# Performance work log

Hardware: AMD Instinct MI355X
Metric: run time of the kernel (lower is better)

## Reference

```python
import jax, jax.numpy as jnp
import numpy as np

DIM = 256
H_GLOBAL = 8
H_LOCAL = 4  # max(1, num_heads // 2)
WINDOW = 5
HALF = WINDOW // 2
B, S = 4, 2048
EPS = 1e-5


def layer_norm(x, g, b):
    mu = jnp.mean(x, axis=-1, keepdims=True)
    var = jnp.mean(jnp.square(x - mu), axis=-1, keepdims=True)
    return (x - mu) * jax.lax.rsqrt(var + EPS) * g + b


def qkv_proj(x, in_w, in_b):
    qkv = x @ in_w.T + in_b
    return jnp.split(qkv, 3, axis=-1)


def global_mha(x, in_w, in_b, out_w, out_b, nh):
    Bq, Sq, D = x.shape
    hd = D // nh
    q, k, v = qkv_proj(x, in_w, in_b)
    q = q.reshape(Bq, Sq, nh, hd)
    k = k.reshape(Bq, Sq, nh, hd)
    v = v.reshape(Bq, Sq, nh, hd)
    scores = jnp.einsum('bqhd,bkhd->bhqk', q, k) / np.sqrt(hd).astype(np.float32)
    attn = jax.nn.softmax(scores, axis=-1)
    o = jnp.einsum('bhqk,bkhd->bqhd', attn, v).reshape(Bq, Sq, D)
    return o @ out_w.T + out_b


def local_mha(x, in_w, in_b, out_w, out_b, nh):
    # banded sliding-window attention, window = 2*HALF+1, per-query softmax
    Bq, Sq, D = x.shape
    hd = D // nh
    q, k, v = qkv_proj(x, in_w, in_b)
    kp = jnp.pad(k, ((0, 0), (HALF, HALF), (0, 0)))
    vp = jnp.pad(v, ((0, 0), (HALF, HALF), (0, 0)))
    # [B, S, W, D] windows of keys/values around each query position
    k_win = jnp.stack([kp[:, j:j + Sq] for j in range(WINDOW)], axis=2)
    v_win = jnp.stack([vp[:, j:j + Sq] for j in range(WINDOW)], axis=2)
    q = q.reshape(Bq, Sq, nh, hd)
    k_win = k_win.reshape(Bq, Sq, WINDOW, nh, hd)
    v_win = v_win.reshape(Bq, Sq, WINDOW, nh, hd)
    scores = jnp.einsum('bshd,bswhd->bshw', q, k_win) / np.sqrt(hd).astype(np.float32)
    idx = jnp.arange(Sq)[:, None] + jnp.arange(-HALF, HALF + 1)[None, :]  # [S, W]
    valid = (idx >= 0) & (idx < Sq)
    scores = jnp.where(valid[None, :, None, :], scores, -jnp.inf)
    attn = jax.nn.softmax(scores, axis=-1)
    o = jnp.einsum('bshw,bswhd->bshd', attn, v_win).reshape(Bq, Sq, D)
    return o @ out_w.T + out_b


def setup_inputs() -> dict:
    key = jax.random.key(0)
    ks = jax.random.split(key, 8)
    sc = 0.02
    d = DIM
    return {
        'x': jax.random.normal(ks[0], (B, S, d), jnp.float32),
        'g_in_w': jax.random.normal(ks[1], (3 * d, d), jnp.float32) * sc,
        'g_in_b': jnp.zeros((3 * d,), jnp.float32),
        'g_out_w': jax.random.normal(ks[2], (d, d), jnp.float32) * sc,
        'g_out_b': jnp.zeros((d,), jnp.float32),
        't_in_w': jax.random.normal(ks[3], (3 * d, d), jnp.float32) * sc,
        't_in_b': jnp.zeros((3 * d,), jnp.float32),
        't_out_w': jax.random.normal(ks[4], (d, d), jnp.float32) * sc,
        't_out_b': jnp.zeros((d,), jnp.float32),
        'fus_w1': jax.random.normal(ks[5], (2 * d, 2 * d), jnp.float32) * sc,
        'fus_b1': jnp.zeros((2 * d,), jnp.float32),
        'fus_w2': jax.random.normal(ks[6], (d, 2 * d), jnp.float32) * sc,
        'fus_b2': jnp.zeros((d,), jnp.float32),
        'ffn_w1': jax.random.normal(ks[7], (2 * d, d), jnp.float32) * sc,
        'ffn_b1': jnp.zeros((2 * d,), jnp.float32),
        'ffn_w2': jax.random.normal(jax.random.fold_in(key, 9), (d, 2 * d), jnp.float32) * sc,
        'ffn_b2': jnp.zeros((d,), jnp.float32),
        'gn_g': jnp.ones((d,), jnp.float32),
        'gn_b': jnp.zeros((d,), jnp.float32),
        'fn_g': jnp.ones((d,), jnp.float32),
        'fn_b': jnp.zeros((d,), jnp.float32),
    }


def reference(x, g_in_w, g_in_b, g_out_w, g_out_b,
              t_in_w, t_in_b, t_out_w, t_out_b,
              fus_w1, fus_b1, fus_w2, fus_b2,
              ffn_w1, ffn_b1, ffn_w2, ffn_b2,
              gn_g, gn_b, fn_g, fn_b):
    x_global = global_mha(x, g_in_w, g_in_b, g_out_w, g_out_b, H_GLOBAL)
    x_local = local_mha(x, t_in_w, t_in_b, t_out_w, t_out_b, H_LOCAL)
    x_comb = jnp.concatenate([x_global, x_local], axis=-1)
    x_fused = jax.nn.silu(x_comb @ fus_w1.T + fus_b1) @ fus_w2.T + fus_b2
    x = layer_norm(x + x_fused, gn_g, gn_b)
    x_ffn = jax.nn.silu(x @ ffn_w1.T + ffn_b1) @ ffn_w2.T + ffn_b2
    x = layer_norm(x + x_ffn, fn_g, fn_b)
    return x
```

## Files before the change

### kernel.cpp

```cpp
#include <hip/hip_runtime.h>

constexpr int Bb = 4;
constexpr int Ss = 2048;
constexpr int QSTR = 1536;

typedef __bf16 bf16x8 __attribute__((ext_vector_type(8)));
typedef __bf16 bf16x4 __attribute__((ext_vector_type(4)));
typedef float  f32x4  __attribute__((ext_vector_type(4)));

__device__ __forceinline__ void glds16(const void* g, void* l) {
    __builtin_amdgcn_global_load_lds(
        (const __attribute__((address_space(1))) unsigned int*)g,
        (__attribute__((address_space(3))) unsigned int*)l, 16, 0, 0);
}

struct CvtArgs {
    const float* src[9];
    __bf16* dst[9];
    int start[10];
};

__global__ __launch_bounds__(256) void convert_all(CvtArgs a)
{
    int e = 0;
    const int bid = blockIdx.x;
#pragma unroll
    for (int i = 0; i < 8; i++) if (bid >= a.start[i + 1]) e = i + 1;
    const int idx = (bid - a.start[e]) * 256 + threadIdx.x;
    const float* s = a.src[e];
    float4 v0 = *(const float4*)&s[(size_t)idx * 8];
    float4 v1 = *(const float4*)&s[(size_t)idx * 8 + 4];
    bf16x8 o;
    o[0] = (__bf16)v0.x; o[1] = (__bf16)v0.y; o[2] = (__bf16)v0.z; o[3] = (__bf16)v0.w;
    o[4] = (__bf16)v1.x; o[5] = (__bf16)v1.y; o[6] = (__bf16)v1.z; o[7] = (__bf16)v1.w;
    *(bf16x8*)&a.dst[e][(size_t)idx * 8] = o;
}

__global__ __launch_bounds__(256) void gemm128(
    const __bf16* __restrict__ A, const __bf16* __restrict__ W,
    const float* __restrict__ bias, const float* __restrict__ bias2, int bsplit,
    __bf16* __restrict__ C, int K, int ldc)
{
    __shared__ __bf16 As[128 * 64];
    __shared__ __bf16 Ws[128 * 64];
    const int tid = threadIdx.x;
    const int lane = tid & 63;
    const int wv = tid >> 6;
    const int wm = (wv >> 1) * 64;
    const int wn = (wv & 1) * 64;
    const int qrow = lane & 15;
    const int quad = lane >> 4;
    const int n0 = blockIdx.x * 128;
    const int m0 = blockIdx.y * 128;

    f32x4 acc[4][4];
#pragma unroll
    for (int i = 0; i < 4; i++)
#pragma unroll
        for (int j = 0; j < 4; j++) acc[i][j] = {0.f, 0.f, 0.f, 0.f};

    for (int k0 = 0; k0 < K; k0 += 64) {
        __syncthreads();
#pragma unroll
        for (int i = 0; i < 4; i++) {
            const int c = (wv * 4 + i) * 64 + lane;
            const int row = c >> 3, g = c & 7;
            const int gs = (g ^ (row & 7)) * 8;
            glds16(&A[(size_t)(m0 + row) * K + k0 + gs], &As[(wv * 4 + i) * 512]);
            glds16(&W[(size_t)(n0 + row) * K + k0 + gs], &Ws[(wv * 4 + i) * 512]);
        }
        __syncthreads();
#pragma unroll
        for (int ksub = 0; ksub < 2; ksub++) {
            const int gl = ksub * 4 + quad;
            bf16x8 af[4], bf[4];
#pragma unroll
            for (int mi = 0; mi < 4; mi++) {
                const int row = wm + mi * 16 + qrow;
                af[mi] = *(const bf16x8*)&As[row * 64 + (gl ^ (row & 7)) * 8];
            }
#pragma unroll
            for (int ni = 0; ni < 4; ni++) {
                const int row = wn + ni * 16 + qrow;
                bf[ni] = *(const bf16x8*)&Ws[row * 64 + (gl ^ (row & 7)) * 8];
            }
#pragma unroll
            for (int mi = 0; mi < 4; mi++)
#pragma unroll
                for (int ni = 0; ni < 4; ni++)
                    acc[mi][ni] = __builtin_amdgcn_mfma_f32_16x16x32_bf16(
                        af[mi], bf[ni], acc[mi][ni], 0, 0, 0);
        }
    }

    float bz[4];
#pragma unroll
    for (int ni = 0; ni < 4; ni++) {
        const int n = n0 + wn + ni * 16 + qrow;
        bz[ni] = (n < bsplit) ? bias[n] : bias2[n - bsplit];
    }
#pragma unroll
    for (int mi = 0; mi < 4; mi++)
#pragma unroll
        for (int r = 0; r < 4; r++) {
            const int row = m0 + wm + mi * 16 + quad * 4 + r;
#pragma unroll
            for (int ni = 0; ni < 4; ni++) {
                float v = acc[mi][ni][r] + bz[ni];
                C[(size_t)row * ldc + n0 + wn + ni * 16 + qrow] = (__bf16)v;
            }
        }
}

template<bool SILU, bool OUT_BF16>
__global__ __launch_bounds__(256) void gemm_small(
    const __bf16* __restrict__ A0, const __bf16* __restrict__ W0,
    const float* __restrict__ bias0, const __bf16* __restrict__ W1,
    const float* __restrict__ bias1, int nsplit, int aoff1, int coff1,
    void* __restrict__ C, int lda, int K, int ldc)
{
    __shared__ __bf16 As[32 * 128];
    __shared__ __bf16 Ws[64 * 128];
    const int tid = threadIdx.x;
    const int lane = tid & 63;
    const int wv = tid >> 6;
    const int wm = (wv >> 1) * 16;
    const int wn = (wv & 1) * 32;
    const int qrow = lane & 15;
    const int quad = lane >> 4;
    const bool second = (int)blockIdx.x >= nsplit;
    const int bx = second ? (blockIdx.x - nsplit) : blockIdx.x;
    const __bf16* A = second ? (A0 + aoff1) : A0;
    const __bf16* W = second ? W1 : W0;
    const float* bias = second ? bias1 : bias0;
    const int coff = second ? coff1 : 0;
    const int n0 = bx * 64;
    const int m0 = blockIdx.y * 32;

    f32x4 acc[2];
    acc[0] = {0.f, 0.f, 0.f, 0.f};
    acc[1] = {0.f, 0.f, 0.f, 0.f};

    for (int k0 = 0; k0 < K; k0 += 128) {
        __syncthreads();
#pragma unroll
        for (int i = 0; i < 2; i++) {
            const int c = (wv * 2 + i) * 64 + lane;
            const int row = c >> 4, s = c & 15;
            const int gs = ((s & 8) | ((s ^ row) & 7)) * 8;
            glds16(&A[(size_t)(m0 + row) * lda + k0 + gs], &As[(wv * 2 + i) * 512]);
        }
#pragma unroll
        for (int i = 0; i < 4; i++) {
            const int c = (wv * 4 + i) * 64 + lane;
            const int row = c >> 4, s = c & 15;
            const int gs = ((s & 8) | ((s ^ row) & 7)) * 8;
            glds16(&W[(size_t)(n0 + row) * K + k0 + gs], &Ws[(wv * 4 + i) * 512]);
        }
        __syncthreads();
#pragma unroll
        for (int ksub = 0; ksub < 4; ksub++) {
            const int gl = ksub * 4 + quad;
            bf16x8 af, bf[2];
            {
                const int row = wm + qrow;
                const int s = (gl & 8) | ((gl ^ row) & 7);
                af = *(const bf16x8*)&As[row * 128 + s * 8];
            }
#pragma unroll
            for (int ni = 0; ni < 2; ni++) {
                const int row = wn + ni * 16 + qrow;
                const int s = (gl & 8) | ((gl ^ row) & 7);
                bf[ni] = *(const bf16x8*)&Ws[row * 128 + s * 8];
            }
#pragma unroll
            for (int ni = 0; ni < 2; ni++)
                acc[ni] = __builtin_amdgcn_mfma_f32_16x16x32_bf16(
                    af, bf[ni], acc[ni], 0, 0, 0);
        }
    }

    float bz[2];
#pragma unroll
    for (int ni = 0; ni < 2; ni++) bz[ni] = bias[n0 + wn + ni * 16 + qrow];

#pragma unroll
    for (int r = 0; r < 4; r++) {
        const int row = m0 + wm + quad * 4 + r;
#pragma unroll
        for (int ni = 0; ni < 2; ni++) {
            float v = acc[ni][r] + bz[ni];
            if (SILU) v = v / (1.f + __expf(-v));
            const int col = coff + n0 + wn + ni * 16 + qrow;
            if (OUT_BF16)
                ((__bf16*)C)[(size_t)row * ldc + col] = (__bf16)v;
            else
                ((float*)C)[(size_t)row * ldc + col] = v;
        }
    }
}

__global__ __launch_bounds__(512) void attn_fused(
    const __bf16* __restrict__ qkv, __bf16* __restrict__ Op,
    float* __restrict__ Lp, __bf16* __restrict__ acat)
{
    __shared__ __bf16 Kl[2][64 * 32];
    __shared__ __bf16 Vt[2][32 * 72];
    __shared__ __bf16 Pl[8][16 * 72];

    const int t = threadIdx.x;
    const int lane = t & 63;
    const int wv = t >> 6;

    if (blockIdx.x < 1024) {
        const int bid = blockIdx.x;
        const int sp = bid & 1;
        const int qc = (bid >> 1) & 15;
        const int h  = (bid >> 5) & 7;
        const int b  = bid >> 8;
        const int bS = b * Ss;
        const int q0 = qc * 128;

        const int qrow = lane & 15;
        const int quad = lane >> 4;
        const float cQ = 1.4426950408889634f * 0.17677669529663687f;

        bf16x8 qf;
        {
            bf16x8 qraw = *(const bf16x8*)(qkv +
                (size_t)(bS + q0 + wv * 16 + qrow) * QSTR + h * 32 + quad * 8);
#pragma unroll
            for (int i = 0; i < 8; i++) qf[i] = (__bf16)((float)qraw[i] * cQ);
        }
        bf16x8 ones;
#pragma unroll
        for (int i = 0; i < 8; i++) ones[i] = (__bf16)1.0f;

        f32x4 o0 = {0.f, 0.f, 0.f, 0.f};
        f32x4 o1 = {0.f, 0.f, 0.f, 0.f};
        f32x4 lac = {0.f, 0.f, 0.f, 0.f};
        const f32x4 z = {0.f, 0.f, 0.f, 0.f};

        const int kc_c = wv * 64 + lane;
        const int kkey = kc_c >> 2, kdg = kc_c & 3;
        const int vkey = t & 63, vq = t >> 6;
        const int kc0 = sp * 16;

        bf16x4 vreg = *(const bf16x4*)(qkv +
            (size_t)(bS + kc0 * 64 + vkey) * QSTR + 512 + h * 32 + vq * 4);
        if (wv < 4)
            glds16(qkv + (size_t)(bS + kc0 * 64 + kkey) * QSTR + 256 + h * 32 + kdg * 8,
                   &Kl[0][wv * 512]);

        for (int i = 0; i < 16; i++) {
            const int cur = i & 1;
#pragma unroll
            for (int e = 0; e < 4; e++) Vt[cur][(vq * 4 + e) * 72 + vkey] = vreg[e];
            __syncthreads();
            const int nx = (i < 15) ? (kc0 + i + 1) : (kc0 + 15);
            vreg = *(const bf16x4*)(qkv +
                (size_t)(bS + nx * 64 + vkey) * QSTR + 512 + h * 32 + vq * 4);
            if (i < 15 && wv < 4)
                glds16(qkv + (size_t)(bS + nx * 64 + kkey) * QSTR + 256 + h * 32 + kdg * 8,
                       &Kl[1 - cur][wv * 512]);

            f32x4 s[4];
#pragma unroll
            for (int kg = 0; kg < 4; kg++) {
                bf16x8 kf = *(const bf16x8*)&Kl[cur][(kg * 16 + qrow) * 32 + quad * 8];
                s[kg] = __builtin_amdgcn_mfma_f32_16x16x32_bf16(kf, qf, z, 0, 0, 0);
            }
#pragma unroll
            for (int kg = 0; kg < 4; kg++) {
                bf16x4 pk;
                pk[0] = (__bf16)exp2f(s[kg][0]);
                pk[1] = (__bf16)exp2f(s[kg][1]);
                pk[2] = (__bf16)exp2f(s[kg][2]);
                pk[3] = (__bf16)exp2f(s[kg][3]);
                *(bf16x4*)&Pl[wv][qrow * 72 + kg * 16 + quad * 4] = pk;
            }
            bf16x8 pf0 = *(const bf16x8*)&Pl[wv][qrow * 72 + quad * 8];
            bf16x8 pf1 = *(const bf16x8*)&Pl[wv][qrow * 72 + 32 + quad * 8];
            bf16x8 vf00 = *(const bf16x8*)&Vt[cur][qrow * 72 + quad * 8];
            bf16x8 vf01 = *(const bf16x8*)&Vt[cur][qrow * 72 + 32 + quad * 8];
            bf16x8 vf10 = *(const bf16x8*)&Vt[cur][(16 + qrow) * 72 + quad * 8];
            bf16x8 vf11 = *(const bf16x8*)&Vt[cur][(16 + qrow) * 72 + 32 + quad * 8];
            o0 = __builtin_amdgcn_mfma_f32_16x16x32_bf16(vf00, pf0, o0, 0, 0, 0);
            o1 = __builtin_amdgcn_mfma_f32_16x16x32_bf16(vf10, pf0, o1, 0, 0, 0);
            lac = __builtin_amdgcn_mfma_f32_16x16x32_bf16(ones, pf0, lac, 0, 0, 0);
            o0 = __builtin_amdgcn_mfma_f32_16x16x32_bf16(vf01, pf1, o0, 0, 0, 0);
            o1 = __builtin_amdgcn_mfma_f32_16x16x32_bf16(vf11, pf1, o1, 0, 0, 0);
            lac = __builtin_amdgcn_mfma_f32_16x16x32_bf16(ones, pf1, lac, 0, 0, 0);
        }

        const int gid = (b * 8 + h) * 2048 + q0 + wv * 16 + qrow;
        __bf16* po = Op + (size_t)sp * 2097152 + (size_t)gid * 32;
        bf16x4 w0, w1;
#pragma unroll
        for (int r = 0; r < 4; r++) { w0[r] = (__bf16)o0[r]; w1[r] = (__bf16)o1[r]; }
        *(bf16x4*)&po[quad * 4]      = w0;
        *(bf16x4*)&po[16 + quad * 4] = w1;
        if (quad == 0) Lp[sp * 65536 + gid] = lac[0];
    } else {
        const int w = (blockIdx.x - 1024) * 8 + wv;
        const int b = w >> 13;
        const int rem = w & 8191;
        const int s = rem >> 2;
        const int h = rem & 3;

        const float q = (float)qkv[(size_t)(b * Ss + s) * QSTR + 768 + h * 64 + lane];
        float sc[5], vv[5];
#pragma unroll
        for (int j = 0; j < 5; j++) {
            int pos = s + j - 2;
            bool valid = (pos >= 0) && (pos < Ss);
            int cpos = valid ? pos : 0;
            const size_t rb = (size_t)(b * Ss + cpos) * QSTR;
            float kj = valid ? (float)qkv[rb + 1024 + h * 64 + lane] : 0.f;
            vv[j] = valid ? (float)qkv[rb + 1280 + h * 64 + lane] : 0.f;
            float p = q * kj;
#pragma unroll
            for (int off = 32; off > 0; off >>= 1) p += __shfl_xor(p, off, 64);
            sc[j] = valid ? p * 0.125f : -1e30f;
        }
        float m = sc[0];
#pragma unroll
        for (int j = 1; j < 5; j++) m = fmaxf(m, sc[j]);
        float l = 0.f, o = 0.f;
#pragma unroll
        for (int j = 0; j < 5; j++) {
            float p = __expf(sc[j] - m);
            l += p; o += p * vv[j];
        }
        acat[(size_t)(b * Ss + s) * 512 + 256 + h * 64 + lane] = (__bf16)(o / l);
    }
}

__global__ __launch_bounds__(256) void attn_combine(
    const __bf16* __restrict__ Op, const float* __restrict__ Lp,
    __bf16* __restrict__ acat)
{
    const int t = blockIdx.x * 256 + threadIdx.x;
    const int gid = t >> 3;
    const int dg = t & 7;
    const int b = gid >> 14;
    const int h = (gid >> 11) & 7;
    const int q = gid & 2047;

    const float li = 1.f / (Lp[gid] + Lp[65536 + gid]);
    const __bf16* base = Op + (size_t)gid * 32 + dg * 4;
    bf16x4 a0 = *(const bf16x4*)&base[0];
    bf16x4 a1 = *(const bf16x4*)&base[2097152];
    bf16x4 r;
#pragma unroll
    for (int i = 0; i < 4; i++)
        r[i] = (__bf16)(((float)a0[i] + (float)a1[i]) * li);
    *(bf16x4*)&acat[(size_t)(b * Ss + q) * 512 + h * 32 + dg * 4] = r;
}

__global__ __launch_bounds__(256) void ln_residual(
    const float* __restrict__ a, const __bf16* __restrict__ r,
    const float* __restrict__ g, const float* __restrict__ be,
    float* __restrict__ out, __bf16* __restrict__ ob)
{
    const int lane = threadIdx.x & 63;
    const int tok = blockIdx.x * 4 + (threadIdx.x >> 6);
    float4 xa = ((const float4*)a)[(size_t)tok * 64 + lane];
    bf16x4 xr = *(const bf16x4*)&r[(size_t)tok * 256 + lane * 4];
    float4 x;
    x.x = xa.x + (float)xr[0]; x.y = xa.y + (float)xr[1];
    x.z = xa.z + (float)xr[2]; x.w = xa.w + (float)xr[3];
    float sum = x.x + x.y + x.z + x.w;
#pragma unroll
    for (int off = 32; off > 0; off >>= 1) sum += __shfl_xor(sum, off, 64);
    float mu = sum * (1.f / 256.f);
    float4 c;
    c.x = x.x - mu; c.y = x.y - mu; c.z = x.z - mu; c.w = x.w - mu;
    float sq = c.x * c.x + c.y * c.y + c.z * c.z + c.w * c.w;
#pragma unroll
    for (int off = 32; off > 0; off >>= 1) sq += __shfl_xor(sq, off, 64);
    float rs = rsqrtf(sq * (1.f / 256.f) + 1e-5f);
    float4 gg = ((const float4*)g)[lane];
    float4 bb = ((const float4*)be)[lane];
    float4 o;
    o.x = c.x * rs * gg.x + bb.x; o.y = c.y * rs * gg.y + bb.y;
    o.z = c.z * rs * gg.z + bb.z; o.w = c.w * rs * gg.w + bb.w;
    ((float4*)out)[(size_t)tok * 64 + lane] = o;
    if (ob) {
        bf16x4 hh;
        hh[0] = (__bf16)o.x; hh[1] = (__bf16)o.y; hh[2] = (__bf16)o.z; hh[3] = (__bf16)o.w;
        *(bf16x4*)&ob[(size_t)tok * 256 + lane * 4] = hh;
    }
}

extern "C" void kernel_launch(void* const* d_in, const int* in_sizes, int n_in,
                              void* d_out, int out_size, void* d_ws, size_t ws_size,
                              hipStream_t stream)
{
    const float* x      = (const float*)d_in[0];
    const float* g_in_w = (const float*)d_in[1];
    const float* g_in_b = (const float*)d_in[2];
    const float* g_out_w= (const float*)d_in[3];
    const float* g_out_b= (const float*)d_in[4];
    const float* t_in_w = (const float*)d_in[5];
    const float* t_in_b = (const float*)d_in[6];
    const float* t_out_w= (const float*)d_in[7];
    const float* t_out_b= (const float*)d_in[8];
    const float* fus_w1 = (const float*)d_in[9];
    const float* fus_b1 = (const float*)d_in[10];
    const float* fus_w2 = (const float*)d_in[11];
    const float* fus_b2 = (const float*)d_in[12];
    const float* ffn_w1 = (const float*)d_in[13];
    const float* ffn_b1 = (const float*)d_in[14];
    const float* ffn_w2 = (const float*)d_in[15];
    const float* ffn_b2 = (const float*)d_in[16];
    const float* gn_g   = (const float*)d_in[17];
    const float* gn_b   = (const float*)d_in[18];
    const float* fn_g   = (const float*)d_in[19];
    const float* fn_b   = (const float*)d_in[20];
    float* out = (float*)d_out;
    float* ws  = (float*)d_ws;

    __bf16* xb     = (__bf16*)(ws);
    __bf16* wb     = (__bf16*)(ws + 1048576);
    __bf16* qkvgl  = (__bf16*)(ws + 1638400);
    __bf16* acat   = (__bf16*)(ws + 7929856);
    __bf16* fcomb  = (__bf16*)(ws + 10027008);
    __bf16* h1     = (__bf16*)(ws + 12124160);
    __bf16* xfb    = (__bf16*)(ws + 14221312);
    float*  x2     = ws + 16318464;
    __bf16* x2b    = (__bf16*)(ws + 18415616);
    __bf16* h2     = h1;
    __bf16* xffb   = xfb;
    __bf16* Op = (__bf16*)(ws + 10027008);
    float*  Lp = ws + 18415616;

    __bf16* w_gin  = wb;
    __bf16* w_gout = wb + 393216;
    __bf16* w_tout = wb + 458752;
    __bf16* w_f1   = wb + 524288;
    __bf16* w_f2   = wb + 786432;
    __bf16* w_n1   = wb + 917504;
    __bf16* w_n2   = wb + 1048576;

    CvtArgs ca;
    ca.src[0] = x;      ca.dst[0] = xb;
    ca.src[1] = g_in_w; ca.dst[1] = w_gin;
    ca.src[2] = t_in_w; ca.dst[2] = w_gin + 196608;
    ca.src[3] = g_out_w;ca.dst[3] = w_gout;
    ca.src[4] = t_out_w;ca.dst[4] = w_tout;
    ca.src[5] = fus_w1; ca.dst[5] = w_f1;
    ca.src[6] = fus_w2; ca.dst[6] = w_f2;
    ca.src[7] = ffn_w1; ca.dst[7] = w_n1;
    ca.src[8] = ffn_w2; ca.dst[8] = w_n2;
    int st[10] = {0, 1024, 1120, 1216, 1248, 1280, 1408, 1472, 1536, 1600};
    for (int i = 0; i < 10; i++) ca.start[i] = st[i];

    convert_all<<<dim3(1600), 256, 0, stream>>>(ca);

    gemm128<<<dim3(12, 64), 256, 0, stream>>>(
        xb, w_gin, g_in_b, t_in_b, 768, qkvgl, 256, QSTR);
    attn_fused<<<dim3(5120), 512, 0, stream>>>(qkvgl, Op, Lp, acat);
    attn_combine<<<dim3(2048), 256, 0, stream>>>(Op, Lp, acat);
    gemm_small<false, true><<<dim3(8, 256), 256, 0, stream>>>(
        acat, w_gout, g_out_b, w_tout, t_out_b, 4, 256, 256, fcomb, 512, 256, 512);
    gemm_small<true,  true><<<dim3(8, 256), 256, 0, stream>>>(
        fcomb, w_f1, fus_b1, w_f1, fus_b1, 1 << 30, 0, 0, h1, 512, 512, 512);
    gemm_small<false, true><<<dim3(4, 256), 256, 0, stream>>>(
        h1, w_f2, fus_b2, w_f2, fus_b2, 1 << 30, 0, 0, xfb, 512, 512, 256);
    ln_residual<<<dim3(2048), 256, 0, stream>>>(x, xfb, gn_g, gn_b, x2, x2b);
    gemm_small<true,  true><<<dim3(8, 256), 256, 0, stream>>>(
        x2b, w_n1, ffn_b1, w_n1, ffn_b1, 1 << 30, 0, 0, h2, 256, 256, 512);
    gemm_small<false, true><<<dim3(4, 256), 256, 0, stream>>>(
        h2, w_n2, ffn_b2, w_n2, ffn_b2, 1 << 30, 0, 0, xffb, 512, 512, 256);
    ln_residual<<<dim3(2048), 256, 0, stream>>>(x2, xffb, fn_g, fn_b, out, nullptr);
}
```

Before: 235.1 us.

## Process two query tiles per wave in global attention and vectorize local attention

The global attention blocks now cover 256 queries instead of 128, with each wave handling two 16-query tiles. Each K/V tile loaded into shared memory is therefore reused across twice as many queries, and the global block count halves. The local sliding-window path packs 8 rows per wave, with each lane doing 8-element bf16x8 vector loads and a 3-step shuffle reduction instead of a 6-step one, cutting the local blocks from 4096 to 512. In exchange, registers and shared memory per block rise and there are fewer blocks to fill the GPU.

```diff
diff --git a/kernel.cpp b/kernel.cpp
--- a/kernel.cpp
+++ b/kernel.cpp
@@ -206,39 +206,44 @@
 {
     __shared__ __bf16 Kl[2][64 * 32];
     __shared__ __bf16 Vt[2][32 * 72];
-    __shared__ __bf16 Pl[8][16 * 72];
+    __shared__ __bf16 Pl[8][2][16 * 72];
 
     const int t = threadIdx.x;
     const int lane = t & 63;
     const int wv = t >> 6;
 
-    if (blockIdx.x < 1024) {
+    if (blockIdx.x < 512) {
         const int bid = blockIdx.x;
         const int sp = bid & 1;
-        const int qc = (bid >> 1) & 15;
-        const int h  = (bid >> 5) & 7;
-        const int b  = bid >> 8;
+        const int qc = (bid >> 1) & 7;
+        const int h  = (bid >> 4) & 7;
+        const int b  = bid >> 7;
         const int bS = b * Ss;
-        const int q0 = qc * 128;
+        const int q0 = qc * 256;
 
         const int qrow = lane & 15;
         const int quad = lane >> 4;
         const float cQ = 1.4426950408889634f * 0.17677669529663687f;
 
-        bf16x8 qf;
-        {
+        bf16x8 qf[2];
+#pragma unroll
+        for (int tl = 0; tl < 2; tl++) {
             bf16x8 qraw = *(const bf16x8*)(qkv +
-                (size_t)(bS + q0 + wv * 16 + qrow) * QSTR + h * 32 + quad * 8);
-#pragma unroll
-            for (int i = 0; i < 8; i++) qf[i] = (__bf16)((float)qraw[i] * cQ);
+                (size_t)(bS + q0 + wv * 32 + tl * 16 + qrow) * QSTR + h * 32 + quad * 8);
+#pragma unroll
+            for (int i = 0; i < 8; i++) qf[tl][i] = (__bf16)((float)qraw[i] * cQ);
         }
         bf16x8 ones;
 #pragma unroll
         for (int i = 0; i < 8; i++) ones[i] = (__bf16)1.0f;
 
-        f32x4 o0 = {0.f, 0.f, 0.f, 0.f};
-        f32x4 o1 = {0.f, 0.f, 0.f, 0.f};
-        f32x4 lac = {0.f, 0.f, 0.f, 0.f};
+        f32x4 o0[2], o1[2], lac[2];
+#pragma unroll
+        for (int tl = 0; tl < 2; tl++) {
+            o0[tl] = {0.f, 0.f, 0.f, 0.f};
+            o1[tl] = {0.f, 0.f, 0.f, 0.f};
+            lac[tl] = {0.f, 0.f, 0.f, 0.f};
+        }
         const f32x4 z = {0.f, 0.f, 0.f, 0.f};
 
         const int kc_c = wv * 64 + lane;
@@ -264,75 +269,109 @@
                 glds16(qkv + (size_t)(bS + nx * 64 + kkey) * QSTR + 256 + h * 32 + kdg * 8,
                        &Kl[1 - cur][wv * 512]);
 
-            f32x4 s[4];
-#pragma unroll
-            for (int kg = 0; kg < 4; kg++) {
-                bf16x8 kf = *(const bf16x8*)&Kl[cur][(kg * 16 + qrow) * 32 + quad * 8];
-                s[kg] = __builtin_amdgcn_mfma_f32_16x16x32_bf16(kf, qf, z, 0, 0, 0);
-            }
-#pragma unroll
-            for (int kg = 0; kg < 4; kg++) {
-                bf16x4 pk;
-                pk[0] = (__bf16)exp2f(s[kg][0]);
-                pk[1] = (__bf16)exp2f(s[kg][1]);
-                pk[2] = (__bf16)exp2f(s[kg][2]);
-                pk[3] = (__bf16)exp2f(s[kg][3]);
-                *(bf16x4*)&Pl[wv][qrow * 72 + kg * 16 + quad * 4] = pk;
-            }
-            bf16x8 pf0 = *(const bf16x8*)&Pl[wv][qrow * 72 + quad * 8];
-            bf16x8 pf1 = *(const bf16x8*)&Pl[wv][qrow * 72 + 32 + quad * 8];
+            bf16x8 kf[4];
+#pragma unroll
+            for (int kg = 0; kg < 4; kg++)
+                kf[kg] = *(const bf16x8*)&Kl[cur][(kg * 16 + qrow) * 32 + quad * 8];
             bf16x8 vf00 = *(const bf16x8*)&Vt[cur][qrow * 72 + quad * 8];
             bf16x8 vf01 = *(const bf16x8*)&Vt[cur][qrow * 72 + 32 + quad * 8];
             bf16x8 vf10 = *(const bf16x8*)&Vt[cur][(16 + qrow) * 72 + quad * 8];
             bf16x8 vf11 = *(const bf16x8*)&Vt[cur][(16 + qrow) * 72 + 32 + quad * 8];
-            o0 = __builtin_amdgcn_mfma_f32_16x16x32_bf16(vf00, pf0, o0, 0, 0, 0);
-            o1 = __builtin_amdgcn_mfma_f32_16x16x32_bf16(vf10, pf0, o1, 0, 0, 0);
-            lac = __builtin_amdgcn_mfma_f32_16x16x32_bf16(ones, pf0, lac, 0, 0, 0);
-            o0 = __builtin_amdgcn_mfma_f32_16x16x32_bf16(vf01, pf1, o0, 0, 0, 0);
-            o1 = __builtin_amdgcn_mfma_f32_16x16x32_bf16(vf11, pf1, o1, 0, 0, 0);
-            lac = __builtin_amdgcn_mfma_f32_16x16x32_bf16(ones, pf1, lac, 0, 0, 0);
-        }
-
-        const int gid = (b * 8 + h) * 2048 + q0 + wv * 16 + qrow;
-        __bf16* po = Op + (size_t)sp * 2097152 + (size_t)gid * 32;
-        bf16x4 w0, w1;
-#pragma unroll
-        for (int r = 0; r < 4; r++) { w0[r] = (__bf16)o0[r]; w1[r] = (__bf16)o1[r]; }
-        *(bf16x4*)&po[quad * 4]      = w0;
-        *(bf16x4*)&po[16 + quad * 4] = w1;
-        if (quad == 0) Lp[sp * 65536 + gid] = lac[0];
+
+#pragma unroll
+            for (int tl = 0; tl < 2; tl++) {
+                f32x4 s[4];
+#pragma unroll
+                for (int kg = 0; kg < 4; kg++)
+                    s[kg] = __builtin_amdgcn_mfma_f32_16x16x32_bf16(
+                        kf[kg], qf[tl], z, 0, 0, 0);
+#pragma unroll
+                for (int kg = 0; kg < 4; kg++) {
+                    bf16x4 pk;
+                    pk[0] = (__bf16)exp2f(s[kg][0]);
+                    pk[1] = (__bf16)exp2f(s[kg][1]);
+                    pk[2] = (__bf16)exp2f(s[kg][2]);
+                    pk[3] = (__bf16)exp2f(s[kg][3]);
+                    *(bf16x4*)&Pl[wv][tl][qrow * 72 + kg * 16 + quad * 4] = pk;
+                }
+                bf16x8 pf0 = *(const bf16x8*)&Pl[wv][tl][qrow * 72 + quad * 8];
+                bf16x8 pf1 = *(const bf16x8*)&Pl[wv][tl][qrow * 72 + 32 + quad * 8];
+                o0[tl] = __builtin_amdgcn_mfma_f32_16x16x32_bf16(vf00, pf0, o0[tl], 0, 0, 0);
+                o1[tl] = __builtin_amdgcn_mfma_f32_16x16x32_bf16(vf10, pf0, o1[tl], 0, 0, 0);
+                lac[tl] = __builtin_amdgcn_mfma_f32_16x16x32_bf16(ones, pf0, lac[tl], 0, 0, 0);
+                o0[tl] = __builtin_amdgcn_mfma_f32_16x16x32_bf16(vf01, pf1, o0[tl], 0, 0, 0);
+                o1[tl] = __builtin_amdgcn_mfma_f32_16x16x32_bf16(vf11, pf1, o1[tl], 0, 0, 0);
+                lac[tl] = __builtin_amdgcn_mfma_f32_16x16x32_bf16(ones, pf1, lac[tl], 0, 0, 0);
+            }
+        }
+
+#pragma unroll
+        for (int tl = 0; tl < 2; tl++) {
+            const int gid = (b * 8 + h) * 2048 + q0 + wv * 32 + tl * 16 + qrow;
+            __bf16* po = Op + (size_t)sp * 2097152 + (size_t)gid * 32;
+            bf16x4 w0, w1;
+#pragma unroll
+            for (int r = 0; r < 4; r++) {
+                w0[r] = (__bf16)o0[tl][r];
+                w1[r] = (__bf16)o1[tl][r];
+            }
+            *(bf16x4*)&po[quad * 4]      = w0;
+            *(bf16x4*)&po[16 + quad * 4] = w1;
+            if (quad == 0) Lp[sp * 65536 + gid] = lac[tl][0];
+        }
     } else {
-        const int w = (blockIdx.x - 1024) * 8 + wv;
-        const int b = w >> 13;
-        const int rem = w & 8191;
-        const int s = rem >> 2;
-        const int h = rem & 3;
-
-        const float q = (float)qkv[(size_t)(b * Ss + s) * QSTR + 768 + h * 64 + lane];
-        float sc[5], vv[5];
+        const int w = (blockIdx.x - 512) * 8 + wv;
+        const int g = lane >> 3;
+        const int l8 = lane & 7;
+        const int R = w * 8 + g;
+        const int h = R & 3;
+        const int s = (R >> 2) & 2047;
+        const int b = R >> 13;
+
+        float qv[8];
+        {
+            bf16x8 q8 = *(const bf16x8*)&qkv[(size_t)(b * Ss + s) * QSTR + 768 + h * 64 + l8 * 8];
+#pragma unroll
+            for (int e = 0; e < 8; e++) qv[e] = (float)q8[e];
+        }
+
+        float sc[5];
+        bf16x8 v8[5];
 #pragma unroll
         for (int j = 0; j < 5; j++) {
             int pos = s + j - 2;
             bool valid = (pos >= 0) && (pos < Ss);
             int cpos = valid ? pos : 0;
             const size_t rb = (size_t)(b * Ss + cpos) * QSTR;
-            float kj = valid ? (float)qkv[rb + 1024 + h * 64 + lane] : 0.f;
-            vv[j] = valid ? (float)qkv[rb + 1280 + h * 64 + lane] : 0.f;
-            float p = q * kj;
-#pragma unroll
-            for (int off = 32; off > 0; off >>= 1) p += __shfl_xor(p, off, 64);
+            bf16x8 k8 = *(const bf16x8*)&qkv[rb + 1024 + h * 64 + l8 * 8];
+            v8[j]     = *(const bf16x8*)&qkv[rb + 1280 + h * 64 + l8 * 8];
+            float p = 0.f;
+#pragma unroll
+            for (int e = 0; e < 8; e++) p += qv[e] * (float)k8[e];
+            p += __shfl_xor(p, 1, 64);
+            p += __shfl_xor(p, 2, 64);
+            p += __shfl_xor(p, 4, 64);
             sc[j] = valid ? p * 0.125f : -1e30f;
         }
         float m = sc[0];
 #pragma unroll
         for (int j = 1; j < 5; j++) m = fmaxf(m, sc[j]);
-        float l = 0.f, o = 0.f;
+        float l = 0.f;
+        float o[8];
+#pragma unroll
+        for (int e = 0; e < 8; e++) o[e] = 0.f;
 #pragma unroll
         for (int j = 0; j < 5; j++) {
-            float p = __expf(sc[j] - m);
-            l += p; o += p * vv[j];
-        }
-        acat[(size_t)(b * Ss + s) * 512 + 256 + h * 64 + lane] = (__bf16)(o / l);
+            float pe = __expf(sc[j] - m);
+            l += pe;
+#pragma unroll
+            for (int e = 0; e < 8; e++) o[e] += pe * (float)v8[j][e];
+        }
+        const float li = 1.f / l;
+        bf16x8 r;
+#pragma unroll
+        for (int e = 0; e < 8; e++) r[e] = (__bf16)(o[e] * li);
+        *(bf16x8*)&acat[(size_t)(b * Ss + s) * 512 + 256 + h * 64 + l8 * 8] = r;
     }
 }
 
@@ -460,7 +499,7 @@
 
     gemm128<<<dim3(12, 64), 256, 0, stream>>>(
         xb, w_gin, g_in_b, t_in_b, 768, qkvgl, 256, QSTR);
-    attn_fused<<<dim3(5120), 512, 0, stream>>>(qkvgl, Op, Lp, acat);
+    attn_fused<<<dim3(1024), 512, 0, stream>>>(qkvgl, Op, Lp, acat);
     attn_combine<<<dim3(2048), 256, 0, stream>>>(Op, Lp, acat);
     gemm_small<false, true><<<dim3(8, 256), 256, 0, stream>>>(
         acat, w_gout, g_out_b, w_tout, t_out_b, 4, 256, 256, fcomb, 512, 256, 512);
```

Result: faster. 221.4 us (-5.8%).
